# Performance work log

Measured on AMD Instinct MI355X. Metric: run time of the kernel, lower is better.

## Reference

```python
import jax, jax.numpy as jnp
import numpy as np

CUTOFF = 5.0
LOG2 = float(np.log(2.0))

def ssp(x):
    # shifted softplus: softplus(x) - log(2)
    return jax.nn.softplus(x) - LOG2

def setup_inputs() -> dict:
    key = jax.random.key(0)
    ks = jax.random.split(key, 12)
    Nb, Na, Nnbh = 8, 1024, 64
    A, F, S = 128, 128, 50
    x = jax.random.normal(ks[0], (Nb, Na, A), dtype=jnp.float32)
    r_ij = jax.random.uniform(ks[1], (Nb, Na, Nnbh), dtype=jnp.float32) * 8.0  # some beyond cutoff=5
    neighbors = jax.random.randint(ks[2], (Nb, Na, Nnbh), 0, Na)
    neighbor_mask = (jax.random.uniform(ks[3], (Nb, Na, Nnbh)) > 0.1).astype(jnp.float32)
    f_ij = jax.random.normal(ks[4], (Nb, Na, Nnbh, S), dtype=jnp.float32)
    sc = lambda n: 1.0 / np.sqrt(n)
    W_in2f = jax.random.normal(ks[5], (F, A), dtype=jnp.float32) * sc(A)
    W_f1 = jax.random.normal(ks[6], (F, S), dtype=jnp.float32) * sc(S)
    b_f1 = jnp.zeros((F,), jnp.float32)
    W_f2 = jax.random.normal(ks[7], (F, F), dtype=jnp.float32) * sc(F)
    b_f2 = jnp.zeros((F,), jnp.float32)
    W_f2out = jax.random.normal(ks[8], (A, F), dtype=jnp.float32) * sc(F)
    b_f2out = jnp.zeros((A,), jnp.float32)
    W_dense = jax.random.normal(ks[9], (A, A), dtype=jnp.float32) * sc(A)
    b_dense = jnp.zeros((A,), jnp.float32)
    return {"x": x, "r_ij": r_ij, "neighbors": neighbors, "neighbor_mask": neighbor_mask,
            "f_ij": f_ij, "W_in2f": W_in2f, "W_f1": W_f1, "b_f1": b_f1, "W_f2": W_f2,
            "b_f2": b_f2, "W_f2out": W_f2out, "b_f2out": b_f2out, "W_dense": W_dense,
            "b_dense": b_dense}

def reference(x, r_ij, neighbors, neighbor_mask, f_ij, W_in2f, W_f1, b_f1, W_f2, b_f2,
              W_f2out, b_f2out, W_dense, b_dense):
    # filter network: Dense(S->F, ssp) -> Dense(F->F)
    W = ssp(jnp.einsum('bans,fs->banf', f_ij, W_f1) + b_f1)
    W = jnp.einsum('bang,fg->banf', W, W_f2) + b_f2          # [Nb,Na,Nnbh,F]
    # hard cutoff
    C = (r_ij <= CUTOFF).astype(W.dtype)                      # [Nb,Na,Nnbh]
    W = W * C[..., None]
    # in2f (no bias)
    y = jnp.einsum('bai,fi->baf', x, W_in2f)                  # [Nb,Na,F]
    # gather neighbor features along atom axis
    yg = jax.vmap(lambda yb, nb: yb[nb])(y, neighbors)        # [Nb,Na,Nnbh,F]
    # masked sum over neighbor axis (Aggregate, mean=False)
    v = jnp.sum(yg * W * neighbor_mask[..., None], axis=2)    # [Nb,Na,F]
    # f2out: Dense(F->A) with ssp, then dense: Dense(A->A)
    v = ssp(jnp.einsum('baf,af->ba' + 'f'[0:0] + 'a'[0:0], v, W_f2out).reshape(v.shape[:2] + (W_f2out.shape[0],)) if False else ssp(v @ W_f2out.T + b_f2out))
    out = v @ W_dense.T + b_dense                             # [Nb,Na,A]
    return out
```

## Files before the change

kernel.cpp:

```cpp
#include <hip/hip_runtime.h>
#include <math.h>


#define RCUT  5.0f
#define LOG2F_ 0.69314718055994530942f
#define LOG2E_ 1.44269504088896340736f

typedef __bf16 bf16x8_t __attribute__((ext_vector_type(8)));
typedef float  f32x4_t  __attribute__((ext_vector_type(4)));

static __device__ __forceinline__ float sspf(float x) {
    float e  = exp2f(-LOG2E_ * fabsf(x));
    float lg = log2f(1.0f + e);
    return fmaf(lg, LOG2F_, fmaxf(x, 0.0f) - LOG2F_);
}
static __device__ __forceinline__ unsigned pack2h(__bf16 a, __bf16 b) {
    union { __bf16 h[2]; unsigned u; } un; un.h[0] = a; un.h[1] = b; return un.u;
}
static __device__ __forceinline__ unsigned pack2f(float a, float b) {
    return pack2h((__bf16)a, (__bf16)b);
}

__global__ __launch_bounds__(256) void prep_kernel(
    const float* __restrict__ W1, const float* __restrict__ W2,
    const float* __restrict__ Wb,
    const float* __restrict__ Wc,
    const float* __restrict__ Wf,
    unsigned* __restrict__ prep)
{
    int i = blockIdx.x * 256 + threadIdx.x;
    if (i < 4096) {
        int sw = i >> 10, ft = (i >> 9) & 1, kh = (i >> 8) & 1;
        int sl = (i >> 2) & 63, j = i & 3;
        int sq = sl >> 4, sm = sl & 15;
        int f = 32 * sw + 16 * ft + sm;
        int c = kh * 16 + 4 * sq + j;
        int k0 = 2 * c, k1 = 2 * c + 1;
        float a = (k0 < 50) ? W1[f * 50 + k0] : 0.0f;
        float b = (k1 < 50) ? W1[f * 50 + k1] : 0.0f;
        prep[i] = pack2f(a, b);
    } else if (i < 12288) {
        int s = i - 4096;
        int sw = s >> 11, ft = (s >> 10) & 1, kq = (s >> 8) & 3;
        int sl = (s >> 2) & 63, j = s & 3;
        int sq = sl >> 4, sm = sl & 15;
        int f = 32 * sw + 16 * ft + sm;
        int c = 16 * kq + 4 * sq + j;
        float2 wv = ((const float2*)W2)[f * 64 + c];
        prep[i] = pack2f(wv.x, wv.y);
    } else {
        int s = i - 12288;
        int L = s >> 14;
        int r = s & 16383;
        int hl = r >> 13;
        int e = r & 8191;
        int sw = e >> 11, ft = (e >> 10) & 1, kq = (e >> 8) & 3;
        int sl = (e >> 2) & 63, j = e & 3;
        int sq = sl >> 4, sm = sl & 15;
        int f = 32 * sw + 16 * ft + sm;
        int c = 16 * kq + 4 * sq + j;
        const float* src = (L == 0) ? Wb : (L == 1) ? Wc : Wf;
        float2 wv = ((const float2*)src)[f * 64 + c];
        if (hl == 0) {
            prep[i] = pack2h((__bf16)wv.x, (__bf16)wv.y);
        } else {
            __bf16 h0 = (__bf16)wv.x, h1 = (__bf16)wv.y;
            prep[i] = pack2f(wv.x - (float)h0, wv.y - (float)h1);
        }
    }
}

__global__ __launch_bounds__(256, 4) void k1_kernel(
    const float* __restrict__ x,
    const unsigned* __restrict__ Wh, const unsigned* __restrict__ Wl,
    float* __restrict__ yout)
{
    __shared__ __bf16 Ah[16 * 136];
    __shared__ __bf16 Al[16 * 136];

    const int t = threadIdx.x;
    const int atom0 = (blockIdx.x >> 1) * 16;
    const int fh = blockIdx.x & 1;
    const int w = t >> 6, l = t & 63, m = l & 15, q = l >> 4;

    {
        const float4* A4 = (const float4*)(x + (size_t)atom0 * 128);
        unsigned* AhU = (unsigned*)Ah;
        unsigned* AlU = (unsigned*)Al;
        #pragma unroll
        for (int r = 0; r < 2; ++r) {
            int lin4 = r * 256 + t;
            int a = lin4 >> 5, k4 = lin4 & 31;
            float4 xv = A4[lin4];
            __bf16 h0=(__bf16)xv.x, h1=(__bf16)xv.y, h2=(__bf16)xv.z, h3=(__bf16)xv.w;
            int idx = a * 68 + 2 * k4;
            AhU[idx]     = pack2h(h0, h1);
            AhU[idx + 1] = pack2h(h2, h3);
            AlU[idx]     = pack2f(xv.x - (float)h0, xv.y - (float)h1);
            AlU[idx + 1] = pack2f(xv.z - (float)h2, xv.w - (float)h3);
        }
    }
    __syncthreads();

    const int ftile = fh * 4 + w;
    const int f = 16 * ftile + m;
    f32x4_t acc = {0.f, 0.f, 0.f, 0.f};
    #pragma unroll
    for (int kk = 0; kk < 4; ++kk) {
        int off = m * 136 + 32 * kk + 8 * q;
        bf16x8_t ah = *(const bf16x8_t*)&Ah[off];
        bf16x8_t al = *(const bf16x8_t*)&Al[off];
        int wo = (ftile * 4 + kk) * 256 + l * 4;
        bf16x8_t wh = *(const bf16x8_t*)(Wh + wo);
        bf16x8_t wl = *(const bf16x8_t*)(Wl + wo);
        acc = __builtin_amdgcn_mfma_f32_16x16x32_bf16(ah, wh, acc, 0, 0, 0);
        acc = __builtin_amdgcn_mfma_f32_16x16x32_bf16(ah, wl, acc, 0, 0, 0);
        acc = __builtin_amdgcn_mfma_f32_16x16x32_bf16(al, wh, acc, 0, 0, 0);
    }
    #pragma unroll
    for (int r = 0; r < 4; ++r)
        yout[(size_t)(atom0 + 4 * q + r) * 128 + f] = acc[r];
}

__global__ __launch_bounds__(256, 4) void interaction_kernel(
    const float* __restrict__ rij, const int* __restrict__ nbrs,
    const float* __restrict__ mask, const float* __restrict__ fij,
    const float* __restrict__ b1, const float* __restrict__ b2,
    const unsigned* __restrict__ W1S,
    const unsigned* __restrict__ W2S,
    const float* __restrict__ y, float* __restrict__ v)
{
    __shared__ __bf16 Hh[64 * 136];
    __shared__ __bf16 Hl[64 * 136];

    const int t  = threadIdx.x;
    const int a  = blockIdx.x;
    const int bi = a >> 10;
    const int p0 = a * 64;
    const int w = t >> 6, l = t & 63, m = l & 15, q = l >> 4;
    const int f0 = 32 * w + m;
    const int f1 = f0 + 16;

    float cy0[16], cy1[16];
    #pragma unroll
    for (int i = 0; i < 16; ++i) {
        int mt = i >> 2, r = i & 3;
        int n = 16 * mt + 4 * q + r;
        float rr = rij[p0 + n];
        float cn = (rr <= RCUT) ? mask[p0 + n] : 0.0f;
        int nbv = (bi << 10) + nbrs[p0 + n];
        const float* yrow = y + (size_t)nbv * 128;
        cy0[i] = cn * yrow[f0];
        cy1[i] = cn * yrow[f1];
    }

    {
        const float* frow = fij + (size_t)(p0 + 16 * w + m) * 50;
        float kv[16];
        #pragma unroll
        for (int j2 = 0; j2 < 4; ++j2) {
            float2 xv = *(const float2*)(frow + 8 * q + 2 * j2);
            kv[2 * j2] = xv.x; kv[2 * j2 + 1] = xv.y;
        }
        #pragma unroll
        for (int j2 = 0; j2 < 4; ++j2) {
            int k = 32 + 8 * q + 2 * j2;
            float2 xv = make_float2(0.f, 0.f);
            if (k < 50) xv = *(const float2*)(frow + k);
            kv[8 + 2 * j2] = xv.x; kv[9 + 2 * j2] = xv.y;
        }
        union { __bf16 h[16]; bf16x8_t v8[2]; } uh, ul;
        #pragma unroll
        for (int k = 0; k < 16; ++k) {
            __bf16 hi = (__bf16)kv[k];
            uh.h[k] = hi;
            ul.h[k] = (__bf16)(kv[k] - (float)hi);
        }
        #pragma unroll 2
        for (int ftile = 0; ftile < 8; ++ftile) {
            float bb = b1[16 * ftile + m];
            f32x4_t acch = {bb, bb, bb, bb};
            f32x4_t accl = {0.f, 0.f, 0.f, 0.f};
            bf16x8_t w0 = *(const bf16x8_t*)(W1S + (ftile * 2 + 0) * 256 + l * 4);
            bf16x8_t w1 = *(const bf16x8_t*)(W1S + (ftile * 2 + 1) * 256 + l * 4);
            acch = __builtin_amdgcn_mfma_f32_16x16x32_bf16(uh.v8[0], w0, acch, 0, 0, 0);
            accl = __builtin_amdgcn_mfma_f32_16x16x32_bf16(ul.v8[0], w0, accl, 0, 0, 0);
            acch = __builtin_amdgcn_mfma_f32_16x16x32_bf16(uh.v8[1], w1, acch, 0, 0, 0);
            accl = __builtin_amdgcn_mfma_f32_16x16x32_bf16(ul.v8[1], w1, accl, 0, 0, 0);
            #pragma unroll
            for (int r = 0; r < 4; ++r) {
                int n = 16 * w + 4 * q + r;
                float hv = sspf(acch[r] + accl[r]);
                __bf16 hh = (__bf16)hv;
                Hh[n * 136 + 16 * ftile + m] = hh;
                Hl[n * 136 + 16 * ftile + m] = (__bf16)(hv - (float)hh);
            }
        }
    }
    __syncthreads();

    const float bb2_0 = b2[f0], bb2_1 = b2[f1];
    bf16x8_t w2f0[4], w2f1[4];
    #pragma unroll
    for (int kq = 0; kq < 4; ++kq) {
        w2f0[kq] = *(const bf16x8_t*)(W2S + ((w * 2 + 0) * 4 + kq) * 256 + l * 4);
        w2f1[kq] = *(const bf16x8_t*)(W2S + ((w * 2 + 1) * 4 + kq) * 256 + l * 4);
    }
    float pv0 = 0.0f, pv1 = 0.0f;
    #pragma unroll
    for (int mt = 0; mt < 4; ++mt) {
        f32x4_t a0h = {bb2_0, bb2_0, bb2_0, bb2_0};
        f32x4_t a0l = {0.f, 0.f, 0.f, 0.f};
        f32x4_t a1h = {bb2_1, bb2_1, bb2_1, bb2_1};
        f32x4_t a1l = {0.f, 0.f, 0.f, 0.f};
        #pragma unroll
        for (int kq = 0; kq < 4; ++kq) {
            int hoff = (16 * mt + m) * 136 + 32 * kq + 8 * q;
            bf16x8_t hh = *(const bf16x8_t*)&Hh[hoff];
            bf16x8_t hl = *(const bf16x8_t*)&Hl[hoff];
            a0h = __builtin_amdgcn_mfma_f32_16x16x32_bf16(hh, w2f0[kq], a0h, 0, 0, 0);
            a0l = __builtin_amdgcn_mfma_f32_16x16x32_bf16(hl, w2f0[kq], a0l, 0, 0, 0);
            a1h = __builtin_amdgcn_mfma_f32_16x16x32_bf16(hh, w2f1[kq], a1h, 0, 0, 0);
            a1l = __builtin_amdgcn_mfma_f32_16x16x32_bf16(hl, w2f1[kq], a1l, 0, 0, 0);
        }
        #pragma unroll
        for (int r = 0; r < 4; ++r) {
            float s0 = a0h[r] + a0l[r];
            float s1 = a1h[r] + a1l[r];
            pv0 = fmaf(cy0[mt * 4 + r], s0, pv0);
            pv1 = fmaf(cy1[mt * 4 + r], s1, pv1);
        }
    }
    pv0 += __shfl_xor(pv0, 16);
    pv0 += __shfl_xor(pv0, 32);
    pv1 += __shfl_xor(pv1, 16);
    pv1 += __shfl_xor(pv1, 32);
    if (l < 16) {
        v[(size_t)a * 128 + f0] = pv0;
        v[(size_t)a * 128 + f1] = pv1;
    }
}

__global__ __launch_bounds__(256, 4) void mgemm2_kernel(
    const float* A,
    const unsigned* __restrict__ W1h, const unsigned* __restrict__ W1l,
    const float* __restrict__ bias1, int nssp1,
    const unsigned* __restrict__ W2h, const unsigned* __restrict__ W2l,
    const float* __restrict__ bias2, int nssp2,
    float* C)
{
    extern __shared__ float smf[];
    __bf16* Ah = (__bf16*)smf;
    __bf16* Al = (__bf16*)(smf + 1088);
    unsigned* AhU = (unsigned*)Ah;
    unsigned* AlU = (unsigned*)Al;

    const int t = threadIdx.x;
    const int atom0 = blockIdx.x * 16;
    const int w = t >> 6, l = t & 63, m = l & 15, q = l >> 4;

    {
        const float4* A4 = (const float4*)(A + (size_t)atom0 * 128);
        #pragma unroll
        for (int r = 0; r < 2; ++r) {
            int lin4 = r * 256 + t;
            int a = lin4 >> 5, k4 = lin4 & 31;
            float4 xv = A4[lin4];
            __bf16 h0=(__bf16)xv.x, h1=(__bf16)xv.y, h2=(__bf16)xv.z, h3=(__bf16)xv.w;
            int idx = a * 68 + 2 * k4;
            AhU[idx]     = pack2h(h0, h1);
            AhU[idx + 1] = pack2h(h2, h3);
            AlU[idx]     = pack2f(xv.x - (float)h0, xv.y - (float)h1);
            AlU[idx + 1] = pack2f(xv.z - (float)h2, xv.w - (float)h3);
        }
    }
    __syncthreads();

    bf16x8_t ah[4], al[4];
    #pragma unroll
    for (int kk = 0; kk < 4; ++kk) {
        int off = m * 136 + 32 * kk + 8 * q;
        ah[kk] = *(const bf16x8_t*)&Ah[off];
        al[kk] = *(const bf16x8_t*)&Al[off];
    }
    f32x4_t acc[2];
    int fidx[2];
    #pragma unroll
    for (int ft = 0; ft < 2; ++ft) {
        fidx[ft] = 16 * (2 * w + ft) + m;
        float b = bias1 ? bias1[fidx[ft]] : 0.0f;
        acc[ft] = (f32x4_t){b, b, b, b};
    }
    #pragma unroll
    for (int ft = 0; ft < 2; ++ft) {
        #pragma unroll
        for (int kk = 0; kk < 4; ++kk) {
            int wo = ((2 * w + ft) * 4 + kk) * 256 + l * 4;
            bf16x8_t wh = *(const bf16x8_t*)(W1h + wo);
            bf16x8_t wl = *(const bf16x8_t*)(W1l + wo);
            acc[ft] = __builtin_amdgcn_mfma_f32_16x16x32_bf16(ah[kk], wh, acc[ft], 0, 0, 0);
            acc[ft] = __builtin_amdgcn_mfma_f32_16x16x32_bf16(ah[kk], wl, acc[ft], 0, 0, 0);
            acc[ft] = __builtin_amdgcn_mfma_f32_16x16x32_bf16(al[kk], wh, acc[ft], 0, 0, 0);
        }
    }
    #pragma unroll
    for (int ft = 0; ft < 2; ++ft)
        #pragma unroll
        for (int r = 0; r < 4; ++r) {
            float o = acc[ft][r];
            if (nssp1 >= 1) o = sspf(o);
            if (nssp1 >= 2) o = sspf(o);
            acc[ft][r] = o;
        }

    __syncthreads();
    #pragma unroll
    for (int ft = 0; ft < 2; ++ft)
        #pragma unroll
        for (int r = 0; r < 4; ++r) {
            float o = acc[ft][r];
            __bf16 hh = (__bf16)o;
            Ah[(4 * q + r) * 136 + fidx[ft]] = hh;
            Al[(4 * q + r) * 136 + fidx[ft]] = (__bf16)(o - (float)hh);
        }
    __syncthreads();

    #pragma unroll
    for (int kk = 0; kk < 4; ++kk) {
        int off = m * 136 + 32 * kk + 8 * q;
        ah[kk] = *(const bf16x8_t*)&Ah[off];
        al[kk] = *(const bf16x8_t*)&Al[off];
    }
    #pragma unroll
    for (int ft = 0; ft < 2; ++ft) {
        float b = bias2 ? bias2[fidx[ft]] : 0.0f;
        acc[ft] = (f32x4_t){b, b, b, b};
    }
    #pragma unroll
    for (int ft = 0; ft < 2; ++ft) {
        #pragma unroll
        for (int kk = 0; kk < 4; ++kk) {
            int wo = ((2 * w + ft) * 4 + kk) * 256 + l * 4;
            bf16x8_t wh = *(const bf16x8_t*)(W2h + wo);
            bf16x8_t wl = *(const bf16x8_t*)(W2l + wo);
            acc[ft] = __builtin_amdgcn_mfma_f32_16x16x32_bf16(ah[kk], wh, acc[ft], 0, 0, 0);
            acc[ft] = __builtin_amdgcn_mfma_f32_16x16x32_bf16(ah[kk], wl, acc[ft], 0, 0, 0);
            acc[ft] = __builtin_amdgcn_mfma_f32_16x16x32_bf16(al[kk], wh, acc[ft], 0, 0, 0);
        }
    }
    #pragma unroll
    for (int ft = 0; ft < 2; ++ft)
        #pragma unroll
        for (int r = 0; r < 4; ++r) {
            float o = acc[ft][r];
            if (nssp2 >= 1) o = sspf(o);
            if (nssp2 >= 2) o = sspf(o);
            C[(size_t)(atom0 + 4 * q + r) * 128 + fidx[ft]] = o;
        }
}

extern "C" void kernel_launch(void* const* d_in, const int* in_sizes, int n_in,
                              void* d_out, int out_size, void* d_ws, size_t ws_size,
                              hipStream_t stream) {
    const float* x        = (const float*)d_in[0];
    const float* rij      = (const float*)d_in[1];
    const int*   nbrs     = (const int*)  d_in[2];
    const float* mask     = (const float*)d_in[3];
    const float* fij      = (const float*)d_in[4];
    const float* W_in2f   = (const float*)d_in[5];
    const float* W_f1     = (const float*)d_in[6];
    const float* b_f1     = (const float*)d_in[7];
    const float* W_f2     = (const float*)d_in[8];
    const float* b_f2     = (const float*)d_in[9];
    const float* W_f2out  = (const float*)d_in[10];
    const float* b_f2out  = (const float*)d_in[11];
    const float* W_dense  = (const float*)d_in[12];
    const float* b_dense  = (const float*)d_in[13];
    float* out = (float*)d_out;

    float*    y    = (float*)d_ws;
    unsigned* prep = (unsigned*)((char*)d_ws + (4u << 20));
    const unsigned* W1S    = prep;
    const unsigned* W2S    = prep + 4096;
    const unsigned* f2o_h  = prep + 12288, *f2o_l  = prep + 20480;
    const unsigned* den_h  = prep + 28672, *den_l  = prep + 36864;
    const unsigned* in2f_h = prep + 45056, *in2f_l = prep + 53248;

    const int MG2_LDS = 2176 * 4;

    prep_kernel<<<240, 256, 0, stream>>>(W_f1, W_f2, W_f2out, W_dense, W_in2f, prep);
    k1_kernel<<<1024, 256, 0, stream>>>(x, in2f_h, in2f_l, y);
    interaction_kernel<<<8192, 256, 0, stream>>>(
        rij, nbrs, mask, fij, b_f1, b_f2, W1S, W2S, y, out);
    mgemm2_kernel<<<512, 256, MG2_LDS, stream>>>(
        out, f2o_h, f2o_l, b_f2out, 2, den_h, den_l, b_dense, 0, out);
}
```

Before: 283.9 us.

## Repartition filter GEMM by neighbor rows per wave and reduce across waves

The second filter GEMM now gives each wave its own 16-neighbor row block and all 128 output features, instead of giving each wave a 32-feature slice over all 64 neighbors. Each wave reads only H rows it wrote itself, so the barrier between the two GEMM stages is removed. The neighbor gathers of y are issued earlier so they overlap with the first GEMM. Per-wave partial sums are then combined through a small shared-memory reduction with one barrier at the end. The cost is higher register pressure (32 gathered y values plus 8 accumulators) and repeated loads of W2 fragments from global memory inside the loop.

Result: faster. 276.1 us (-2.8%).

```diff
diff --git a/kernel.cpp b/kernel.cpp
--- a/kernel.cpp
+++ b/kernel.cpp
@@ -132,49 +132,54 @@
 {
     __shared__ __bf16 Hh[64 * 136];
     __shared__ __bf16 Hl[64 * 136];
+    __shared__ float  red[512];
 
     const int t  = threadIdx.x;
     const int a  = blockIdx.x;
     const int bi = a >> 10;
     const int p0 = a * 64;
     const int w = t >> 6, l = t & 63, m = l & 15, q = l >> 4;
-    const int f0 = 32 * w + m;
-    const int f1 = f0 + 16;
-
-    float cy0[16], cy1[16];
-    #pragma unroll
-    for (int i = 0; i < 16; ++i) {
-        int mt = i >> 2, r = i & 3;
-        int n = 16 * mt + 4 * q + r;
-        float rr = rij[p0 + n];
-        float cn = (rr <= RCUT) ? mask[p0 + n] : 0.0f;
-        int nbv = (bi << 10) + nbrs[p0 + n];
-        const float* yrow = y + (size_t)nbv * 128;
-        cy0[i] = cn * yrow[f0];
-        cy1[i] = cn * yrow[f1];
+
+    const float* frow = fij + (size_t)(p0 + 16 * w + m) * 50;
+    float kv[16];
+    #pragma unroll
+    for (int j2 = 0; j2 < 4; ++j2) {
+        float2 xv = *(const float2*)(frow + 8 * q + 2 * j2);
+        kv[2 * j2] = xv.x; kv[2 * j2 + 1] = xv.y;
+    }
+    #pragma unroll
+    for (int j2 = 0; j2 < 4; ++j2) {
+        int k = 32 + 8 * q + 2 * j2;
+        float2 xv = make_float2(0.f, 0.f);
+        if (k < 50) xv = *(const float2*)(frow + k);
+        kv[8 + 2 * j2] = xv.x; kv[9 + 2 * j2] = xv.y;
+    }
+
+    int   nbr_[4];
+    float cb_[4];
+    #pragma unroll
+    for (int r = 0; r < 4; ++r) {
+        int n = p0 + 16 * w + 4 * q + r;
+        float rr = rij[n];
+        cb_[r] = (rr <= RCUT) ? mask[n] : 0.0f;
+        nbr_[r] = (bi << 10) + nbrs[n];
+    }
+    float yv[32];
+    #pragma unroll
+    for (int r = 0; r < 4; ++r) {
+        const float* yrow = y + (size_t)nbr_[r] * 128 + m;
+        #pragma unroll
+        for (int ftB = 0; ftB < 8; ++ftB)
+            yv[r * 8 + ftB] = yrow[16 * ftB];
     }
 
     {
-        const float* frow = fij + (size_t)(p0 + 16 * w + m) * 50;
-        float kv[16];
-        #pragma unroll
-        for (int j2 = 0; j2 < 4; ++j2) {
-            float2 xv = *(const float2*)(frow + 8 * q + 2 * j2);
-            kv[2 * j2] = xv.x; kv[2 * j2 + 1] = xv.y;
-        }
-        #pragma unroll
-        for (int j2 = 0; j2 < 4; ++j2) {
-            int k = 32 + 8 * q + 2 * j2;
-            float2 xv = make_float2(0.f, 0.f);
-            if (k < 50) xv = *(const float2*)(frow + k);
-            kv[8 + 2 * j2] = xv.x; kv[9 + 2 * j2] = xv.y;
-        }
-        union { __bf16 h[16]; bf16x8_t v8[2]; } uh, ul;
+        union { __bf16 e[16]; bf16x8_t v8[2]; } uh, ul;
         #pragma unroll
         for (int k = 0; k < 16; ++k) {
             __bf16 hi = (__bf16)kv[k];
-            uh.h[k] = hi;
-            ul.h[k] = (__bf16)(kv[k] - (float)hi);
+            uh.e[k] = hi;
+            ul.e[k] = (__bf16)(kv[k] - (float)hi);
         }
         #pragma unroll 2
         for (int ftile = 0; ftile < 8; ++ftile) {
@@ -197,47 +202,63 @@
             }
         }
     }
-    __syncthreads();
-
-    const float bb2_0 = b2[f0], bb2_1 = b2[f1];
-    bf16x8_t w2f0[4], w2f1[4];
-    #pragma unroll
-    for (int kq = 0; kq < 4; ++kq) {
-        w2f0[kq] = *(const bf16x8_t*)(W2S + ((w * 2 + 0) * 4 + kq) * 256 + l * 4);
-        w2f1[kq] = *(const bf16x8_t*)(W2S + ((w * 2 + 1) * 4 + kq) * 256 + l * 4);
-    }
-    float pv0 = 0.0f, pv1 = 0.0f;
-    #pragma unroll
-    for (int mt = 0; mt < 4; ++mt) {
-        f32x4_t a0h = {bb2_0, bb2_0, bb2_0, bb2_0};
-        f32x4_t a0l = {0.f, 0.f, 0.f, 0.f};
-        f32x4_t a1h = {bb2_1, bb2_1, bb2_1, bb2_1};
-        f32x4_t a1l = {0.f, 0.f, 0.f, 0.f};
+
+    float cy[32];
+    #pragma unroll
+    for (int r = 0; r < 4; ++r)
+        #pragma unroll
+        for (int ftB = 0; ftB < 8; ++ftB)
+            cy[r * 8 + ftB] = cb_[r] * yv[r * 8 + ftB];
+
+    float partial[8];
+    #pragma unroll
+    for (int h2 = 0; h2 < 2; ++h2) {
+        f32x4_t acch[4], accl[4];
+        #pragma unroll
+        for (int j = 0; j < 4; ++j) {
+            int ftB = 4 * h2 + j;
+            float bb = b2[16 * ftB + m];
+            acch[j] = (f32x4_t){bb, bb, bb, bb};
+            accl[j] = (f32x4_t){0.f, 0.f, 0.f, 0.f};
+        }
         #pragma unroll
         for (int kq = 0; kq < 4; ++kq) {
-            int hoff = (16 * mt + m) * 136 + 32 * kq + 8 * q;
+            int hoff = (16 * w + m) * 136 + 32 * kq + 8 * q;
             bf16x8_t hh = *(const bf16x8_t*)&Hh[hoff];
             bf16x8_t hl = *(const bf16x8_t*)&Hl[hoff];
-            a0h = __builtin_amdgcn_mfma_f32_16x16x32_bf16(hh, w2f0[kq], a0h, 0, 0, 0);
-            a0l = __builtin_amdgcn_mfma_f32_16x16x32_bf16(hl, w2f0[kq], a0l, 0, 0, 0);
-            a1h = __builtin_amdgcn_mfma_f32_16x16x32_bf16(hh, w2f1[kq], a1h, 0, 0, 0);
-            a1l = __builtin_amdgcn_mfma_f32_16x16x32_bf16(hl, w2f1[kq], a1l, 0, 0, 0);
-        }
-        #pragma unroll
-        for (int r = 0; r < 4; ++r) {
-            float s0 = a0h[r] + a0l[r];
-            float s1 = a1h[r] + a1l[r];
-            pv0 = fmaf(cy0[mt * 4 + r], s0, pv0);
-            pv1 = fmaf(cy1[mt * 4 + r], s1, pv1);
-        }
-    }
-    pv0 += __shfl_xor(pv0, 16);
-    pv0 += __shfl_xor(pv0, 32);
-    pv1 += __shfl_xor(pv1, 16);
-    pv1 += __shfl_xor(pv1, 32);
-    if (l < 16) {
-        v[(size_t)a * 128 + f0] = pv0;
-        v[(size_t)a * 128 + f1] = pv1;
+            #pragma unroll
+            for (int j = 0; j < 4; ++j) {
+                int ftB = 4 * h2 + j;
+                bf16x8_t w2 = *(const bf16x8_t*)(W2S + (ftB * 4 + kq) * 256 + l * 4);
+                acch[j] = __builtin_amdgcn_mfma_f32_16x16x32_bf16(hh, w2, acch[j], 0, 0, 0);
+                accl[j] = __builtin_amdgcn_mfma_f32_16x16x32_bf16(hl, w2, accl[j], 0, 0, 0);
+            }
+        }
+        #pragma unroll
+        for (int j = 0; j < 4; ++j) {
+            int ftB = 4 * h2 + j;
+            float s = 0.0f;
+            #pragma unroll
+            for (int r = 0; r < 4; ++r)
+                s = fmaf(cy[r * 8 + ftB], acch[j][r] + accl[j][r], s);
+            partial[ftB] = s;
+        }
+    }
+
+    #pragma unroll
+    for (int ftB = 0; ftB < 8; ++ftB) {
+        partial[ftB] += __shfl_xor(partial[ftB], 16);
+        partial[ftB] += __shfl_xor(partial[ftB], 32);
+    }
+    if (q == 0) {
+        #pragma unroll
+        for (int ftB = 0; ftB < 8; ++ftB)
+            red[w * 128 + 16 * ftB + m] = partial[ftB];
+    }
+    __syncthreads();
+    if (t < 128) {
+        float s = red[t] + red[128 + t] + red[256 + t] + red[384 + t];
+        v[(size_t)a * 128 + t] = s;
     }
 }
 
```
